# Kernel optimization log

Measured on AMD Instinct MI355X. Metric: run time of the kernel, lower is better.

Reference implementation:

```python
import jax, jax.numpy as jnp
import numpy as np

# Module constants (match init_kwargs)
E = 8           # num_experts
K = 2           # num_experts_per_tok
BLOCK = 16      # BLOCK_SIZE hardcoded in module
NORM_TOPK = True


def setup_inputs() -> dict:
    key = jax.random.key(0)
    k0, k1, k2, k3 = jax.random.split(key, 4)
    B, S, H = 2, 2048, 768
    F = 4 * H  # ffn_hidden_size
    x = jax.random.normal(k0, (B, S, H), dtype=jnp.float32)
    router_w = jax.random.normal(k1, (E, H), dtype=jnp.float32) * 0.02
    # kaiming-uniform-ish scale for w1/w2
    w1 = jax.random.uniform(k2, (H, E * F), dtype=jnp.float32, minval=-1.0, maxval=1.0) * float(1.0 / np.sqrt(H))
    w2 = jax.random.uniform(k3, (E * F, H), dtype=jnp.float32, minval=-1.0, maxval=1.0) * float(1.0 / np.sqrt(E * F))
    return {"x": x, "router_w": router_w, "w1": w1, "w2": w2}


def _moe_forward(x, router_w, w1, w2):
    B, S, H = x.shape
    T = B * S
    x_flat = x.reshape(T, H)

    # Router
    router_logits = x_flat @ router_w.T                      # [T, E]
    rw = jax.nn.softmax(router_logits.astype(jnp.float32), axis=-1)
    top_w, sel = jax.lax.top_k(rw, K)                        # [T, K]
    if NORM_TOPK:
        top_w = top_w / top_w.sum(axis=-1, keepdims=True)
    top_w = top_w.astype(x.dtype)  # NOTE: computed but NOT applied in combine (faithful to source)

    # Block-padding multiplicities (faithful to source's duplicate-last-token padding bug):
    # assignments are sorted stably by expert; the LAST assignment of each expert's
    # group is duplicated pad_e = (-count_e) % BLOCK times and then scatter-added.
    sel_flat = sel.reshape(-1)                               # [T*K], token-major stable order
    flat_idx = jnp.arange(T * K, dtype=jnp.int32)
    counts = jax.ops.segment_sum(jnp.ones((T * K,), jnp.int32), sel_flat, num_segments=E)
    pad = (-counts) % BLOCK                                  # [E]
    last_idx = jax.ops.segment_max(flat_idx, sel_flat, num_segments=E)  # [E]
    mult = 1 + jnp.where(flat_idx == last_idx[sel_flat], pad[sel_flat], 0)  # [T*K]

    # Combine coefficients coef[t, e] = multiplicity of (token t, expert e) assignment
    token_ids = flat_idx // K
    coef = jnp.zeros((T, E), dtype=x.dtype).at[token_ids, sel_flat].add(mult.astype(x.dtype))

    # Expert FFNs: y1 = gelu(x @ W1_e) @ W2_e, combined with coef (NOT routing weights)
    F = w1.shape[1] // E
    w1e = w1.reshape(H, E, F)
    w2e = w2.reshape(E, F, H)
    out = jnp.zeros((T, H), dtype=x.dtype)
    for e in range(E):  # small fixed loop over experts
        h = jax.nn.gelu(x_flat @ w1e[:, e, :], approximate=False)  # [T, F]
        out = out + coef[:, e:e + 1] * (h @ w2e[e])                # [T, H]

    return out.reshape(B, S, H), router_logits


def reference(x, router_w, w1, w2):
    return _moe_forward(x, router_w, w1, w2)
```

## Files before the change

kernel.cpp:

```cpp
#include <hip/hip_runtime.h>
#include <math.h>

#define T_TOK 4096
#define H_DIM 768
#define E_NUM 8
#define F_DIM 3072
#define EF_DIM 24576
#define BK 64
#define SEG_MAX 9216
#define MAX_TILES 72

#define OFF_PAD     24
#define OFF_SEG     32
#define OFF_NT      40
#define OFF_TOTAL   41
#define OFF_SCHED_E 48
#define OFF_SCHED_G 120

#define WS_SEL   768
#define WS_TOK   33536
#define WS_COEF  70400
#define WS_XG    107264ull
#define WS_HG    14263040ull
#define WS_WT    70886144ull

typedef __attribute__((ext_vector_type(8))) short short8;
typedef __attribute__((ext_vector_type(4))) float float4v;

__device__ __forceinline__ short f2b(float f) {
  union { float f; unsigned u; } v; v.f = f;
  unsigned r = v.u + 0x7FFFu + ((v.u >> 16) & 1u);
  return (short)(r >> 16);
}
__device__ __forceinline__ float gelu_fast(float v) {
  const float z = 1.5957691216f * fmaf(0.044715f * v * v, v, v);
  return v / (1.0f + __expf(-z));
}
__device__ __forceinline__ void gl_lds16(const void* g, void* l) {
  __builtin_amdgcn_global_load_lds(
      (const __attribute__((address_space(1))) void*)g,
      (__attribute__((address_space(3))) void*)l, 16, 0, 0);
}

__global__ __launch_bounds__(256) void router_k(const float* __restrict__ x,
                                                const float* __restrict__ rw,
                                                float* __restrict__ logits_out,
                                                int* __restrict__ sel) {
  __shared__ float rws[E_NUM * H_DIM];
  for (int i = threadIdx.x; i < E_NUM * H_DIM; i += 256) rws[i] = rw[i];
  __syncthreads();
  const int wid = threadIdx.x >> 6, lane = threadIdx.x & 63;
  const int t = blockIdx.x * 4 + wid;
  const float* xr = x + (size_t)t * H_DIM;
  double acc[E_NUM];
#pragma unroll
  for (int e = 0; e < E_NUM; ++e) acc[e] = 0.0;
  for (int i = 0; i < H_DIM / 64; ++i) {
    const int h = lane + 64 * i;
    const float xv = xr[h];
#pragma unroll
    for (int e = 0; e < E_NUM; ++e) acc[e] += (double)xv * (double)rws[e * H_DIM + h];
  }
#pragma unroll
  for (int e = 0; e < E_NUM; ++e)
    for (int off = 32; off; off >>= 1) acc[e] += __shfl_down(acc[e], off);
  if (lane == 0) {
    float lg[E_NUM];
#pragma unroll
    for (int e = 0; e < E_NUM; ++e) { lg[e] = (float)acc[e]; logits_out[t * E_NUM + e] = lg[e]; }
    int e0 = 0;
    for (int e = 1; e < E_NUM; ++e) if (lg[e] > lg[e0]) e0 = e;
    int e1 = -1;
    for (int e = 0; e < E_NUM; ++e) {
      if (e == e0) continue;
      if (e1 < 0 || lg[e] > lg[e1]) e1 = e;
    }
    sel[t * 2 + 0] = e0;
    sel[t * 2 + 1] = e1;
  }
}

__global__ __launch_bounds__(1024) void setup_k(const int* __restrict__ sel,
                                                int* __restrict__ meta,
                                                int* __restrict__ tok,
                                                float* __restrict__ coefv) {
  __shared__ int cnt_s[E_NUM], last_s[E_NUM], cur_s[E_NUM], seg_s[E_NUM], pad_s[E_NUM];
  const int tid = threadIdx.x;
  const int lane = tid & 63;
  if (tid < E_NUM) { cnt_s[tid] = 0; last_s[tid] = 0; }
  __syncthreads();

  int my_e[8];
#pragma unroll
  for (int it = 0; it < 8; ++it) {
    const int a = it * 1024 + tid;
    const int e_a = sel[a];
    my_e[it] = e_a;
#pragma unroll
    for (int e = 0; e < E_NUM; ++e) {
      const unsigned long long mask = __ballot(e_a == e);
      if (mask) {
        const int leader = (int)__ffsll((long long)mask) - 1;
        if (lane == leader) {
          atomicAdd(&cnt_s[e], (int)__popcll(mask));
          const int hi = 63 - (int)__clzll(mask);
          atomicMax(&last_s[e], (a - lane) + hi + 1);
        }
      }
    }
  }
  __syncthreads();

  if (tid == 0) {
    int s = 0, nt = 0;
    for (int e = 0; e < E_NUM; ++e) {
      const int c = cnt_s[e];
      seg_s[e] = s;
      cur_s[e] = s;
      pad_s[e] = (16 - (c & 15)) & 15;
      meta[OFF_PAD + e] = pad_s[e];
      meta[OFF_SEG + e] = s;
      const int ru = (c + 127) & ~127;
      for (int m = 0; m < ru; m += 128) {
        meta[OFF_SCHED_E + nt] = e;
        meta[OFF_SCHED_G + nt] = s + m;
        ++nt;
      }
      s += ru;
    }
    meta[OFF_NT] = nt;
    meta[OFF_TOTAL] = s;
    for (int k = nt; k < MAX_TILES; ++k) { meta[OFF_SCHED_E + k] = -1; meta[OFF_SCHED_G + k] = 0; }
  }
  __syncthreads();

  for (int e = 0; e < E_NUM; ++e) {
    const int c = cnt_s[e];
    const int ru = (c + 127) & ~127;
    const int sg = seg_s[e];
    for (int p = c + tid; p < ru; p += 1024) { tok[sg + p] = -1; coefv[sg + p] = 0.0f; }
  }
  {
    const int s_all = seg_s[E_NUM - 1] + ((cnt_s[E_NUM - 1] + 127) & ~127);
    for (int p = s_all + tid; p < SEG_MAX; p += 1024) { tok[p] = -1; coefv[p] = 0.0f; }
  }

#pragma unroll
  for (int it = 0; it < 8; ++it) {
    const int a = it * 1024 + tid;
    const int e_a = my_e[it];
#pragma unroll
    for (int e = 0; e < E_NUM; ++e) {
      const unsigned long long mask = __ballot(e_a == e);
      if (e_a == e) {
        const int leader = (int)__ffsll((long long)mask) - 1;
        int base = 0;
        if (lane == leader) base = atomicAdd(&cur_s[e], (int)__popcll(mask));
        base = __shfl(base, leader);
        const int rank = (int)__popcll(mask & ((1ull << lane) - 1ull));
        const int g = base + rank;
        tok[g] = a >> 1;
        coefv[g] = (last_s[e] == a + 1) ? (float)(1 + pad_s[e]) : 1.0f;
      }
    }
  }
}

__global__ __launch_bounds__(256) void gather_x_k(const float* __restrict__ x,
                                                  const int* __restrict__ tok,
                                                  short* __restrict__ xg) {
  const int u = blockIdx.x * 256 + threadIdx.x;
  const int g = u / 96;
  const int c = (u - g * 96) * 8;
  const int t = tok[g];
  short8 v = {0, 0, 0, 0, 0, 0, 0, 0};
  if (t >= 0) {
    const float* src = x + (size_t)t * H_DIM + c;
    float4v f0 = *(const float4v*)src;
    float4v f1 = *(const float4v*)(src + 4);
    v[0] = f2b(f0[0]); v[1] = f2b(f0[1]); v[2] = f2b(f0[2]); v[3] = f2b(f0[3]);
    v[4] = f2b(f1[0]); v[5] = f2b(f1[1]); v[6] = f2b(f1[2]); v[7] = f2b(f1[3]);
  }
  *(short8*)&xg[(size_t)g * H_DIM + c] = v;
}

__global__ __launch_bounds__(256) void conv_w1_k(const float* __restrict__ w1, short* __restrict__ w1t) {
  __shared__ float tile[64][65];
  const int n0 = blockIdx.x * 64;
  const int h0 = blockIdx.y * 64;
  const int tid = threadIdx.x;
  const int rr = tid >> 4;
  const int cc = (tid & 15) * 4;
#pragma unroll
  for (int p = 0; p < 4; ++p) {
    const int r = p * 16 + rr;
    float4v f = *(const float4v*)(w1 + (size_t)(h0 + r) * EF_DIM + n0 + cc);
    tile[r][cc] = f[0]; tile[r][cc + 1] = f[1]; tile[r][cc + 2] = f[2]; tile[r][cc + 3] = f[3];
  }
  __syncthreads();
#pragma unroll
  for (int p = 0; p < 2; ++p) {
    const int item = p * 256 + tid;
    const int nl = item >> 3;
    const int u8 = (item & 7) * 8;
    short8 v;
#pragma unroll
    for (int j = 0; j < 8; ++j) v[j] = f2b(tile[u8 + j][nl]);
    *(short8*)(w1t + (size_t)(n0 + nl) * H_DIM + h0 + u8) = v;
  }
}

__global__ __launch_bounds__(256) void conv_w2_k(const float* __restrict__ w2, short* __restrict__ w2t) {
  __shared__ float tile[64][65];
  const int k0 = blockIdx.x * 64;
  const int h0 = blockIdx.y * 64;
  const int e = k0 / F_DIM;
  const int f0 = k0 - e * F_DIM;
  const int tid = threadIdx.x;
  const int rr = tid >> 4;
  const int cc = (tid & 15) * 4;
#pragma unroll
  for (int p = 0; p < 4; ++p) {
    const int r = p * 16 + rr;
    float4v f = *(const float4v*)(w2 + (size_t)(k0 + r) * H_DIM + h0 + cc);
    tile[r][cc] = f[0]; tile[r][cc + 1] = f[1]; tile[r][cc + 2] = f[2]; tile[r][cc + 3] = f[3];
  }
  __syncthreads();
#pragma unroll
  for (int p = 0; p < 2; ++p) {
    const int item = p * 256 + tid;
    const int nl = item >> 3;
    const int u8 = (item & 7) * 8;
    short8 v;
#pragma unroll
    for (int j = 0; j < 8; ++j) v[j] = f2b(tile[u8 + j][nl]);
    *(short8*)(w2t + (size_t)(e * H_DIM + h0 + nl) * F_DIM + f0 + u8) = v;
  }
}


__global__ __launch_bounds__(256) void gemm1_k(const short* __restrict__ xg,
                                               const short* __restrict__ w1t,
                                               const int* __restrict__ meta,
                                               short* __restrict__ hg) {
  const int slot = blockIdx.y;
  if (slot >= meta[OFF_NT]) return;
  const int e = meta[OFF_SCHED_E + slot];
  const int gbase = meta[OFF_SCHED_G + slot];
  const int n0 = blockIdx.x * 128;

  __shared__ short As[128 * BK];
  __shared__ short Bs[128 * BK];

  const int tid = threadIdx.x;
  const int w = tid >> 6, l = tid & 63;
  const int mw = (w & 1) * 64, nw = (w >> 1) * 64;
  const int lrow = l & 15, q = l >> 4;

  const int srow = l >> 3;
  const int schunk = (l & 7) ^ srow;
  const short* agp[4];
  const short* bgp[4];
  short* alp[4];
  short* blp[4];
#pragma unroll
  for (int i = 0; i < 4; ++i) {
    const int r = i * 32 + w * 8 + srow;
    agp[i] = xg + (size_t)(gbase + r) * H_DIM + schunk * 8;
    bgp[i] = w1t + (size_t)(e * F_DIM + n0 + r) * H_DIM + schunk * 8;
    alp[i] = &As[(i * 32 + w * 8) * BK + l * 8];
    blp[i] = &Bs[(i * 32 + w * 8) * BK + l * 8];
  }
  const int rsw = lrow & 7;

  float4v acc[4][4] = {};

  for (int k0 = 0; k0 < H_DIM; k0 += BK) {
#pragma unroll
    for (int i = 0; i < 4; ++i) gl_lds16(agp[i] + k0, alp[i]);
#pragma unroll
    for (int i = 0; i < 4; ++i) gl_lds16(bgp[i] + k0, blp[i]);
    __syncthreads();
#pragma unroll
    for (int s = 0; s < 2; ++s) {
      short8 a_frag[4], b_frag[4];
      const int csw = ((s * 4 + q) ^ rsw) * 8;
#pragma unroll
      for (int i = 0; i < 4; ++i) a_frag[i] = *(const short8*)&As[(mw + 16 * i + lrow) * BK + csw];
#pragma unroll
      for (int j = 0; j < 4; ++j) b_frag[j] = *(const short8*)&Bs[(nw + 16 * j + lrow) * BK + csw];
#pragma unroll
      for (int i = 0; i < 4; ++i)
#pragma unroll
        for (int j = 0; j < 4; ++j)
          acc[i][j] = __builtin_amdgcn_mfma_f32_16x16x32_bf16(a_frag[i], b_frag[j], acc[i][j], 0, 0, 0);
    }
    __syncthreads();
  }
#pragma unroll
  for (int i = 0; i < 4; ++i)
#pragma unroll
    for (int j = 0; j < 4; ++j)
#pragma unroll
      for (int r = 0; r < 4; ++r) {
        const int row = mw + 16 * i + q * 4 + r;
        const int col = nw + 16 * j + lrow;
        hg[(size_t)(gbase + row) * F_DIM + n0 + col] = f2b(gelu_fast(acc[i][j][r]));
      }
}

__global__ __launch_bounds__(256) void gemm2_k(const short* __restrict__ hg,
                                               const short* __restrict__ w2t,
                                               const int* __restrict__ meta,
                                               const int* __restrict__ tok,
                                               const float* __restrict__ coefv,
                                               float* __restrict__ out) {
  const int slot = blockIdx.y;
  if (slot >= meta[OFF_NT]) return;
  const int e = meta[OFF_SCHED_E + slot];
  const int gbase = meta[OFF_SCHED_G + slot];
  const int n0 = blockIdx.x * 128;
  const int kbase = blockIdx.z * (F_DIM / 2);

  __shared__ short As[128 * BK];
  __shared__ short Bs[128 * BK];

  const int tid = threadIdx.x;
  const int w = tid >> 6, l = tid & 63;
  const int mw = (w & 1) * 64, nw = (w >> 1) * 64;
  const int lrow = l & 15, q = l >> 4;

  const int srow = l >> 3;
  const int schunk = (l & 7) ^ srow;
  const short* agp[4];
  const short* bgp[4];
  short* alp[4];
  short* blp[4];
#pragma unroll
  for (int i = 0; i < 4; ++i) {
    const int r = i * 32 + w * 8 + srow;
    agp[i] = hg + (size_t)(gbase + r) * F_DIM + kbase + schunk * 8;
    bgp[i] = w2t + (size_t)(e * H_DIM + n0 + r) * F_DIM + kbase + schunk * 8;
    alp[i] = &As[(i * 32 + w * 8) * BK + l * 8];
    blp[i] = &Bs[(i * 32 + w * 8) * BK + l * 8];
  }
  const int rsw = lrow & 7;

  float4v acc[4][4] = {};

  for (int k0 = 0; k0 < F_DIM / 2; k0 += BK) {
#pragma unroll
    for (int i = 0; i < 4; ++i) gl_lds16(agp[i] + k0, alp[i]);
#pragma unroll
    for (int i = 0; i < 4; ++i) gl_lds16(bgp[i] + k0, blp[i]);
    __syncthreads();
#pragma unroll
    for (int s = 0; s < 2; ++s) {
      short8 a_frag[4], b_frag[4];
      const int csw = ((s * 4 + q) ^ rsw) * 8;
#pragma unroll
      for (int i = 0; i < 4; ++i) a_frag[i] = *(const short8*)&As[(mw + 16 * i + lrow) * BK + csw];
#pragma unroll
      for (int j = 0; j < 4; ++j) b_frag[j] = *(const short8*)&Bs[(nw + 16 * j + lrow) * BK + csw];
#pragma unroll
      for (int i = 0; i < 4; ++i)
#pragma unroll
        for (int j = 0; j < 4; ++j)
          acc[i][j] = __builtin_amdgcn_mfma_f32_16x16x32_bf16(a_frag[i], b_frag[j], acc[i][j], 0, 0, 0);
    }
    __syncthreads();
  }
#pragma unroll
  for (int i = 0; i < 4; ++i)
#pragma unroll
    for (int r = 0; r < 4; ++r) {
      const int row = mw + 16 * i + q * 4 + r;
      const int g = gbase + row;
      const int t = tok[g];
      if (t < 0) continue;
      const float cf = coefv[g];
#pragma unroll
      for (int j = 0; j < 4; ++j) {
        const int col = nw + 16 * j + lrow;
        atomicAdd(&out[(size_t)t * H_DIM + n0 + col], cf * acc[i][j][r]);
      }
    }
}

extern "C" void kernel_launch(void* const* d_in, const int* in_sizes, int n_in,
                              void* d_out, int out_size, void* d_ws, size_t ws_size,
                              hipStream_t stream) {
  const float* x  = (const float*)d_in[0];
  const float* rw = (const float*)d_in[1];
  const float* w1 = (const float*)d_in[2];
  const float* w2 = (const float*)d_in[3];
  float* out = (float*)d_out;
  float* logits = out + (size_t)T_TOK * H_DIM;

  char* ws = (char*)d_ws;
  int*   meta  = (int*)ws;
  int*   sel   = (int*)(ws + WS_SEL);
  int*   tok   = (int*)(ws + WS_TOK);
  float* coefv = (float*)(ws + WS_COEF);
  short* xg    = (short*)(ws + WS_XG);
  short* hg    = (short*)(ws + WS_HG);
  short* wt    = (short*)(ws + WS_WT);

  hipMemsetAsync(d_out, 0, (size_t)T_TOK * H_DIM * sizeof(float), stream);

  conv_w1_k<<<dim3(EF_DIM / 64, H_DIM / 64), 256, 0, stream>>>(w1, wt);
  router_k<<<T_TOK / 4, 256, 0, stream>>>(x, rw, logits, sel);
  setup_k<<<1, 1024, 0, stream>>>(sel, meta, tok, coefv);
  gather_x_k<<<(SEG_MAX * (H_DIM / 8)) / 256, 256, 0, stream>>>(x, tok, xg);
  gemm1_k<<<dim3(F_DIM / 128, MAX_TILES), 256, 0, stream>>>(xg, wt, meta, hg);
  conv_w2_k<<<dim3(EF_DIM / 64, H_DIM / 64), 256, 0, stream>>>(w2, wt);
  gemm2_k<<<dim3(H_DIM / 128, MAX_TILES, 2), 256, 0, stream>>>(hg, wt, meta, tok, coefv, out);
}
```

Measured before the change: 427.0 us.

## Split single-block routing setup into per-expert histogram and scatter kernels

```diff
diff --git a/kernel.cpp b/kernel.cpp
--- a/kernel.cpp
+++ b/kernel.cpp
@@ -10,8 +10,8 @@
 #define SEG_MAX 9216
 #define MAX_TILES 72
 
-#define OFF_PAD     24
-#define OFF_SEG     32
+#define OFF_CNT      0
+#define OFF_LAST     8
 #define OFF_NT      40
 #define OFF_TOTAL   41
 #define OFF_SCHED_E 48
@@ -80,89 +80,91 @@
   }
 }
 
-__global__ __launch_bounds__(1024) void setup_k(const int* __restrict__ sel,
-                                                int* __restrict__ meta,
-                                                int* __restrict__ tok,
-                                                float* __restrict__ coefv) {
-  __shared__ int cnt_s[E_NUM], last_s[E_NUM], cur_s[E_NUM], seg_s[E_NUM], pad_s[E_NUM];
-  const int tid = threadIdx.x;
-  const int lane = tid & 63;
-  if (tid < E_NUM) { cnt_s[tid] = 0; last_s[tid] = 0; }
-  __syncthreads();
-
-  int my_e[8];
+__global__ __launch_bounds__(1024) void hist_k(const int* __restrict__ sel,
+                                               int* __restrict__ meta) {
+  const int e = blockIdx.x;
+  const int tid = threadIdx.x, lane = tid & 63, wid = tid >> 6;
+  __shared__ int wcnt[16], wlast[16];
+  int c = 0, lmax = 0;
 #pragma unroll
   for (int it = 0; it < 8; ++it) {
     const int a = it * 1024 + tid;
-    const int e_a = sel[a];
-    my_e[it] = e_a;
-#pragma unroll
-    for (int e = 0; e < E_NUM; ++e) {
-      const unsigned long long mask = __ballot(e_a == e);
-      if (mask) {
-        const int leader = (int)__ffsll((long long)mask) - 1;
-        if (lane == leader) {
-          atomicAdd(&cnt_s[e], (int)__popcll(mask));
-          const int hi = 63 - (int)__clzll(mask);
-          atomicMax(&last_s[e], (a - lane) + hi + 1);
-        }
-      }
-    }
-  }
+    const unsigned long long mask = __ballot(sel[a] == e);
+    if (lane == 0 && mask) {
+      c += (int)__popcll(mask);
+      const int hi = 63 - (int)__clzll((long long)mask);
+      const int cand = a + hi + 1;
+      lmax = lmax > cand ? lmax : cand;
+    }
+  }
+  if (lane == 0) { wcnt[wid] = c; wlast[wid] = lmax; }
   __syncthreads();
-
   if (tid == 0) {
-    int s = 0, nt = 0;
-    for (int e = 0; e < E_NUM; ++e) {
-      const int c = cnt_s[e];
-      seg_s[e] = s;
-      cur_s[e] = s;
-      pad_s[e] = (16 - (c & 15)) & 15;
-      meta[OFF_PAD + e] = pad_s[e];
-      meta[OFF_SEG + e] = s;
-      const int ru = (c + 127) & ~127;
-      for (int m = 0; m < ru; m += 128) {
-        meta[OFF_SCHED_E + nt] = e;
-        meta[OFF_SCHED_G + nt] = s + m;
+    int C = 0, L = 0;
+    for (int w = 0; w < 16; ++w) { C += wcnt[w]; L = L > wlast[w] ? L : wlast[w]; }
+    meta[OFF_CNT + e] = C;
+    meta[OFF_LAST + e] = L;
+  }
+}
+
+__global__ __launch_bounds__(1024) void scatter_k(const int* __restrict__ sel,
+                                                  int* __restrict__ meta,
+                                                  int* __restrict__ tok,
+                                                  float* __restrict__ coefv) {
+  const int e = blockIdx.x;
+  const int tid = threadIdx.x, lane = tid & 63, wid = tid >> 6;
+  __shared__ int wv[16];
+
+  int cnt[E_NUM];
+#pragma unroll
+  for (int i = 0; i < E_NUM; ++i) cnt[i] = meta[OFF_CNT + i];
+  int seg = 0;
+  for (int i = 0; i < e; ++i) seg += (cnt[i] + 127) & ~127;
+  const int c = cnt[e];
+  const int ru = (c + 127) & ~127;
+  const int pad = (16 - (c & 15)) & 15;
+  const int laste = meta[OFF_LAST + e];
+  const float lastcoef = (float)(1 + pad);
+
+  for (int p = c + tid; p < ru; p += 1024) { tok[seg + p] = -1; coefv[seg + p] = 0.0f; }
+  if (e == E_NUM - 1) {
+    const int total = seg + ru;
+    for (int p = total + tid; p < SEG_MAX; p += 1024) { tok[p] = -1; coefv[p] = 0.0f; }
+  }
+
+  if (e == 0) {
+    int nt = 0, s2 = 0;
+    for (int i = 0; i < E_NUM; ++i) {
+      const int rui = (cnt[i] + 127) & ~127;
+      for (int m = 0; m < rui; m += 128) {
+        if (nt == tid) { meta[OFF_SCHED_E + nt] = i; meta[OFF_SCHED_G + nt] = s2 + m; }
         ++nt;
       }
-      s += ru;
-    }
-    meta[OFF_NT] = nt;
-    meta[OFF_TOTAL] = s;
-    for (int k = nt; k < MAX_TILES; ++k) { meta[OFF_SCHED_E + k] = -1; meta[OFF_SCHED_G + k] = 0; }
-  }
-  __syncthreads();
-
-  for (int e = 0; e < E_NUM; ++e) {
-    const int c = cnt_s[e];
-    const int ru = (c + 127) & ~127;
-    const int sg = seg_s[e];
-    for (int p = c + tid; p < ru; p += 1024) { tok[sg + p] = -1; coefv[sg + p] = 0.0f; }
-  }
-  {
-    const int s_all = seg_s[E_NUM - 1] + ((cnt_s[E_NUM - 1] + 127) & ~127);
-    for (int p = s_all + tid; p < SEG_MAX; p += 1024) { tok[p] = -1; coefv[p] = 0.0f; }
-  }
-
+      s2 += rui;
+    }
+    if (tid >= nt && tid < MAX_TILES) { meta[OFF_SCHED_E + tid] = -1; meta[OFF_SCHED_G + tid] = 0; }
+    if (tid == 0) { meta[OFF_NT] = nt; meta[OFF_TOTAL] = s2; }
+  }
+
+  int running = 0;
 #pragma unroll
   for (int it = 0; it < 8; ++it) {
     const int a = it * 1024 + tid;
-    const int e_a = my_e[it];
-#pragma unroll
-    for (int e = 0; e < E_NUM; ++e) {
-      const unsigned long long mask = __ballot(e_a == e);
-      if (e_a == e) {
-        const int leader = (int)__ffsll((long long)mask) - 1;
-        int base = 0;
-        if (lane == leader) base = atomicAdd(&cur_s[e], (int)__popcll(mask));
-        base = __shfl(base, leader);
-        const int rank = (int)__popcll(mask & ((1ull << lane) - 1ull));
-        const int g = base + rank;
-        tok[g] = a >> 1;
-        coefv[g] = (last_s[e] == a + 1) ? (float)(1 + pad_s[e]) : 1.0f;
-      }
-    }
+    const bool f = (sel[a] == e);
+    const unsigned long long mask = __ballot(f);
+    if (lane == 0) wv[wid] = (int)__popcll(mask);
+    __syncthreads();
+    int pre = 0, tot = 0;
+#pragma unroll
+    for (int w = 0; w < 16; ++w) { const int v = wv[w]; pre += (w < wid) ? v : 0; tot += v; }
+    if (f) {
+      const int rank = (int)__popcll(mask & ((1ull << lane) - 1ull));
+      const int g = seg + running + pre + rank;
+      tok[g] = a >> 1;
+      coefv[g] = (laste == a + 1) ? lastcoef : 1.0f;
+    }
+    running += tot;
+    __syncthreads();
   }
 }
 
@@ -410,7 +412,8 @@
 
   conv_w1_k<<<dim3(EF_DIM / 64, H_DIM / 64), 256, 0, stream>>>(w1, wt);
   router_k<<<T_TOK / 4, 256, 0, stream>>>(x, rw, logits, sel);
-  setup_k<<<1, 1024, 0, stream>>>(sel, meta, tok, coefv);
+  hist_k<<<E_NUM, 1024, 0, stream>>>(sel, meta);
+  scatter_k<<<E_NUM, 1024, 0, stream>>>(sel, meta, tok, coefv);
   gather_x_k<<<(SEG_MAX * (H_DIM / 8)) / 256, 256, 0, stream>>>(x, tok, xg);
   gemm1_k<<<dim3(F_DIM / 128, MAX_TILES), 256, 0, stream>>>(xg, wt, meta, hg);
   conv_w2_k<<<dim3(EF_DIM / 64, H_DIM / 64), 256, 0, stream>>>(w2, wt);
```

Measured after the change: 390.6 us. 8.5% less time.
